# Kernel optimization log

Measured on AMD Instinct MI355X. Metric: run time of the kernel, lower is better.

Reference implementation:

```python
import jax, jax.numpy as jnp
import numpy as np

N_NODES = 100000
N_EDGES = 1600000
C = 64       # in_channels == filters
K = 3        # Chebyshev order
EPS = 1e-5   # InstanceNorm eps


def setup_inputs() -> dict:
    key = jax.random.key(0)
    ks = jax.random.split(key, 8)
    x = jax.random.normal(ks[0], (N_NODES, C), dtype=jnp.float32)
    edge_index = jax.random.randint(ks[1], (2, N_EDGES), 0, N_NODES, dtype=jnp.int64)
    scale = 1.0 / np.sqrt(C)
    W1 = jax.random.normal(ks[2], (K, C, C), dtype=jnp.float32) * scale
    b1 = jnp.zeros((C,), dtype=jnp.float32)
    W2 = jax.random.normal(ks[3], (K, C, C), dtype=jnp.float32) * scale
    b2 = jnp.zeros((C,), dtype=jnp.float32)
    return {"x": x, "edge_index": edge_index, "W1": W1, "b1": b1, "W2": W2, "b2": b2}


def _cheb_conv(x, src, dst, w_edge, W, b, n):
    # PyG ChebConv, norm='sym', lambda_max=2: L_hat = -D^{-1/2} A D^{-1/2}
    def prop(h):  # h: [N, C] -> L_hat @ h via gather -> weight -> scatter-add
        return jax.ops.segment_sum(w_edge[:, None] * h[src], dst, num_segments=n)
    Tx0 = x
    Tx1 = prop(x)
    Tx2 = 2.0 * prop(Tx1) - Tx0
    return Tx0 @ W[0] + Tx1 @ W[1] + Tx2 @ W[2] + b


def _instance_norm(h):
    # PyG InstanceNorm (single graph, affine=False): normalize over nodes per channel
    m = h.mean(axis=0, keepdims=True)
    v = h.var(axis=0, keepdims=True)
    return (h - m) * jax.lax.rsqrt(v + EPS)


def reference(x, edge_index, W1, b1, W2, b2):
    n = x.shape[0]
    src, dst = edge_index[0], edge_index[1]
    ones = jnp.ones((src.shape[0],), dtype=x.dtype)
    deg = jax.ops.segment_sum(ones, dst, num_segments=n)
    safe = jnp.where(deg > 0, deg, 1.0)
    dinv = jnp.where(deg > 0, jax.lax.rsqrt(safe), 0.0)
    w_edge = -dinv[src] * dinv[dst]  # scaled-Laplacian edge weights
    h = _instance_norm(jax.nn.relu(_cheb_conv(x, src, dst, w_edge, W1, b1, n)))
    h = _instance_norm(jax.nn.relu(_cheb_conv(h, src, dst, w_edge, W2, b2, n)))
    return h
```

## Files before the change

### kernel.cpp

```cpp
#include <hip/hip_runtime.h>
#include <hip/hip_fp16.h>

#define NCH 64
#define EPS 1e-5f
#define SBANKS 32
#define BSHIFT 8
#define NHIST 256
#define BINCAP 6400
#define SRCMASK 0x1FFFFu
#define QW_SCALE 32767.0f
#define QW_INV (1.0f/32767.0f)

typedef _Float16 f16x8 __attribute__((ext_vector_type(8)));
typedef float f32x4 __attribute__((ext_vector_type(4)));

__global__ __launch_bounds__(256) void k_front(const float* __restrict__ x, __half* __restrict__ xh,
                                               int castTotal, int castB,
                                               const float* __restrict__ W1, _Float16* __restrict__ Wb1,
                                               const float* __restrict__ W2, _Float16* __restrict__ Wb2,
                                               const int* __restrict__ dst, int* __restrict__ cnt,
                                               int E, int per, int nbuck) {
    int bid = blockIdx.x;
    if (bid < castB) {
        int i = (bid * 256 + threadIdx.x) * 4;
        if (i < castTotal) {
            float4 f = *(const float4*)(x + i);
            __half2* o = (__half2*)(xh + i);
            o[0] = __floats2half2_rn(f.x, f.y);
            o[1] = __floats2half2_rn(f.z, f.w);
        }
        return;
    }
    if (bid < castB + 96) {
        int wb = bid - castB;
        const float* W = (wb < 48) ? W1 : W2;
        _Float16* Wb = (wb < 48) ? Wb1 : Wb2;
        int idx = (wb % 48) * 256 + threadIdx.x;
        int j = idx & 7;
        int lane = (idx >> 3) & 63;
        int tk = idx >> 9;
        int tile = tk / 6, kk = tk % 6;
        int k = kk * 32 + (lane >> 4) * 8 + j;
        int n = tile * 16 + (lane & 15);
        Wb[idx] = (_Float16)W[k * 64 + n];
        return;
    }
    __shared__ int lh[512];
    int hb = bid - castB - 96;
    for (int t = threadIdx.x; t < nbuck; t += 256) lh[t] = 0;
    __syncthreads();
    int lo = hb * per, hi = min(E, lo + per);
    for (int e = lo + threadIdx.x; e < hi; e += 256)
        atomicAdd(&lh[dst[e] >> BSHIFT], 1);
    __syncthreads();
    for (int t = threadIdx.x; t < nbuck; t += 256)
        if (lh[t]) atomicAdd(&cnt[t], lh[t]);
}

__global__ void k_bscan(const int* __restrict__ cnt, int* __restrict__ gbase,
                        int* __restrict__ gcur, int nbuck, int E) {
    __shared__ int s[512];
    int t = threadIdx.x;
    int v = (t < nbuck) ? cnt[t] : 0;
    s[t] = v;
    __syncthreads();
    for (int off = 1; off < 512; off <<= 1) {
        int add = (t >= off) ? s[t - off] : 0;
        __syncthreads();
        s[t] += add;
        __syncthreads();
    }
    if (t < nbuck) { int ex = s[t] - v; gbase[t] = ex; gcur[t] = ex; }
    if (t == 0) gbase[nbuck] = E;
}

__global__ __launch_bounds__(256) void k_bin(const int* __restrict__ src,
                                             const int* __restrict__ dst,
                                             int* __restrict__ gcur,
                                             int2* __restrict__ binned, int E, int per, int nbuck) {
    __shared__ int lh[512];
    __shared__ int lsc[512];
    __shared__ int lbase[512];
    __shared__ int lcur[512];
    __shared__ int2 sedge[BINCAP];
    int t = threadIdx.x;
    for (int i = t; i < 512; i += 256) lh[i] = 0;
    __syncthreads();
    int lo = blockIdx.x * per, hi = min(E, lo + per);
    for (int e = lo + t; e < hi; e += 256)
        atomicAdd(&lh[dst[e] >> BSHIFT], 1);
    __syncthreads();
    int v0 = lh[t], v1 = lh[t + 256];
    lsc[t] = v0; lsc[t + 256] = v1;
    __syncthreads();
    for (int off = 1; off < 512; off <<= 1) {
        int a0 = (t >= off) ? lsc[t - off] : 0;
        int a1 = (t + 256 >= off) ? lsc[t + 256 - off] : 0;
        __syncthreads();
        lsc[t] += a0; lsc[t + 256] += a1;
        __syncthreads();
    }
    lsc[t] -= v0; lsc[t + 256] -= v1;
    if (t < nbuck && v0) lbase[t] = atomicAdd(&gcur[t], v0);
    if (t + 256 < nbuck && v1) lbase[t + 256] = atomicAdd(&gcur[t + 256], v1);
    lcur[t] = lsc[t]; lcur[t + 256] = lsc[t + 256];
    __syncthreads();
    for (int e = lo + t; e < hi; e += 256) {
        int d = dst[e];
        int b = d >> BSHIFT;
        int pos = atomicAdd(&lcur[b], 1);
        sedge[pos] = make_int2(src[e], d);
    }
    __syncthreads();
    int cntE = hi - lo;
    for (int i = t; i < cntE; i += 256) {
        int2 sd = sedge[i];
        int b = sd.y >> BSHIFT;
        binned[lbase[b] + (i - lsc[b])] = sd;
    }
}

__global__ __launch_bounds__(256) void k_bucket(const int2* __restrict__ binned,
                                                const int* __restrict__ gbase,
                                                float* __restrict__ dinv,
                                                int* __restrict__ rowstart,
                                                unsigned int* __restrict__ csr, int N, int nbuck, int E) {
    __shared__ int hist[256];
    __shared__ int lcur[256];
    __shared__ int ltmp[256];
    int b = blockIdx.x;
    int t = threadIdx.x;
    int nodeLo = b << BSHIFT;
    int nHere = min(256, N - nodeLo);
    int e0 = gbase[b], e1 = gbase[b + 1];
    hist[t] = 0;
    __syncthreads();
    for (int e = e0 + t; e < e1; e += 256)
        atomicAdd(&hist[binned[e].y - nodeLo], 1);
    __syncthreads();
    int deg = (t < nHere) ? hist[t] : 0;
    if (t < nHere) dinv[nodeLo + t] = (deg > 0) ? rsqrtf((float)deg) : 0.0f;
    ltmp[t] = deg;
    __syncthreads();
    for (int off = 1; off < 256; off <<= 1) {
        int add = (t >= off) ? ltmp[t - off] : 0;
        __syncthreads();
        ltmp[t] += add;
        __syncthreads();
    }
    int lstart = ltmp[t] - deg;
    if (t < nHere) rowstart[nodeLo + t] = e0 + lstart;
    if (b == nbuck - 1 && t == 0) rowstart[N] = E;
    lcur[t] = lstart;
    __syncthreads();
    for (int e = e0 + t; e < e1; e += 256) {
        int2 sd = binned[e];
        int dl = sd.y - nodeLo;
        int pos = atomicAdd(&lcur[dl], 1);
        unsigned int dd = (unsigned int)min(hist[dl], 32767);
        csr[e0 + pos] = (unsigned int)sd.x | (dd << 17);
    }
}

__global__ void k_weights(unsigned int* __restrict__ csr, const float* __restrict__ dinv, int E) {
    int e = blockIdx.x * blockDim.x + threadIdx.x;
    if (e < E) {
        unsigned int v = csr[e];
        unsigned int s = v & SRCMASK;
        float dd = rsqrtf((float)(v >> 17));
        float aw = dinv[s] * dd;
        unsigned int qw = (unsigned int)(aw * QW_SCALE + 0.5f);
        csr[e] = s | (qw << 17);
    }
}

__device__ __forceinline__ void edge_acc(const __half* __restrict__ h, unsigned int v,
                                         int li, float& sw, float (&acc)[8]) {
    uint4 a = *(const uint4*)(h + (size_t)(v & SRCMASK) * NCH + li * 8);
    float w = -(float)(v >> 17) * QW_INV;
    sw += w;
    float2 f;
    f = __half22float2(*(__half2*)&a.x); acc[0] = fmaf(w, f.x, acc[0]); acc[1] = fmaf(w, f.y, acc[1]);
    f = __half22float2(*(__half2*)&a.y); acc[2] = fmaf(w, f.x, acc[2]); acc[3] = fmaf(w, f.y, acc[3]);
    f = __half22float2(*(__half2*)&a.z); acc[4] = fmaf(w, f.x, acc[4]); acc[5] = fmaf(w, f.y, acc[5]);
    f = __half22float2(*(__half2*)&a.w); acc[6] = fmaf(w, f.x, acc[6]); acc[7] = fmaf(w, f.y, acc[7]);
}

__global__ __launch_bounds__(256) void k_prop(const __half* __restrict__ h,
                                              const int* __restrict__ rowstart,
                                              const unsigned int* __restrict__ csr,
                                              const __half* __restrict__ tx0,
                                              __half* __restrict__ y, int N,
                                              const float* __restrict__ gstats,
                                              const float* __restrict__ tstats) {
    int lane = threadIdx.x & 63;
    int wv = (blockIdx.x * 256 + threadIdx.x) >> 6;
    int g = lane >> 3, li = lane & 7;
    int node = wv * 8 + g;
    int e = 0, e1 = 0;
    if (node < N) { e = rowstart[node]; e1 = rowstart[node + 1]; }
    float acc[8] = {0.f, 0.f, 0.f, 0.f, 0.f, 0.f, 0.f, 0.f};
    float sw = 0.0f;
    for (; e + 4 <= e1; e += 4) {
        unsigned int v0 = csr[e], v1 = csr[e + 1], v2 = csr[e + 2], v3 = csr[e + 3];
        uint4 a0 = *(const uint4*)(h + (size_t)(v0 & SRCMASK) * NCH + li * 8);
        uint4 a1 = *(const uint4*)(h + (size_t)(v1 & SRCMASK) * NCH + li * 8);
        uint4 a2 = *(const uint4*)(h + (size_t)(v2 & SRCMASK) * NCH + li * 8);
        uint4 a3 = *(const uint4*)(h + (size_t)(v3 & SRCMASK) * NCH + li * 8);
        float w0 = -(float)(v0 >> 17) * QW_INV;
        float w1 = -(float)(v1 >> 17) * QW_INV;
        float w2 = -(float)(v2 >> 17) * QW_INV;
        float w3 = -(float)(v3 >> 17) * QW_INV;
        sw += (w0 + w1) + (w2 + w3);
        float2 f;
        f = __half22float2(*(__half2*)&a0.x); acc[0] = fmaf(w0, f.x, acc[0]); acc[1] = fmaf(w0, f.y, acc[1]);
        f = __half22float2(*(__half2*)&a0.y); acc[2] = fmaf(w0, f.x, acc[2]); acc[3] = fmaf(w0, f.y, acc[3]);
        f = __half22float2(*(__half2*)&a0.z); acc[4] = fmaf(w0, f.x, acc[4]); acc[5] = fmaf(w0, f.y, acc[5]);
        f = __half22float2(*(__half2*)&a0.w); acc[6] = fmaf(w0, f.x, acc[6]); acc[7] = fmaf(w0, f.y, acc[7]);
        f = __half22float2(*(__half2*)&a1.x); acc[0] = fmaf(w1, f.x, acc[0]); acc[1] = fmaf(w1, f.y, acc[1]);
        f = __half22float2(*(__half2*)&a1.y); acc[2] = fmaf(w1, f.x, acc[2]); acc[3] = fmaf(w1, f.y, acc[3]);
        f = __half22float2(*(__half2*)&a1.z); acc[4] = fmaf(w1, f.x, acc[4]); acc[5] = fmaf(w1, f.y, acc[5]);
        f = __half22float2(*(__half2*)&a1.w); acc[6] = fmaf(w1, f.x, acc[6]); acc[7] = fmaf(w1, f.y, acc[7]);
        f = __half22float2(*(__half2*)&a2.x); acc[0] = fmaf(w2, f.x, acc[0]); acc[1] = fmaf(w2, f.y, acc[1]);
        f = __half22float2(*(__half2*)&a2.y); acc[2] = fmaf(w2, f.x, acc[2]); acc[3] = fmaf(w2, f.y, acc[3]);
        f = __half22float2(*(__half2*)&a2.z); acc[4] = fmaf(w2, f.x, acc[4]); acc[5] = fmaf(w2, f.y, acc[5]);
        f = __half22float2(*(__half2*)&a2.w); acc[6] = fmaf(w2, f.x, acc[6]); acc[7] = fmaf(w2, f.y, acc[7]);
        f = __half22float2(*(__half2*)&a3.x); acc[0] = fmaf(w3, f.x, acc[0]); acc[1] = fmaf(w3, f.y, acc[1]);
        f = __half22float2(*(__half2*)&a3.y); acc[2] = fmaf(w3, f.x, acc[2]); acc[3] = fmaf(w3, f.y, acc[3]);
        f = __half22float2(*(__half2*)&a3.z); acc[4] = fmaf(w3, f.x, acc[4]); acc[5] = fmaf(w3, f.y, acc[5]);
        f = __half22float2(*(__half2*)&a3.w); acc[6] = fmaf(w3, f.x, acc[6]); acc[7] = fmaf(w3, f.y, acc[7]);
    }
    for (; e < e1; e++) {
        unsigned int v = csr[e];
        edge_acc(h, v, li, sw, acc);
    }
    if (node >= N) return;
    if (gstats != nullptr) {
        float4 m0 = *(const float4*)(gstats + li * 8);
        float4 m1 = *(const float4*)(gstats + li * 8 + 4);
        float4 r0 = *(const float4*)(gstats + 64 + li * 8);
        float4 r1 = *(const float4*)(gstats + 64 + li * 8 + 4);
        acc[0] = r0.x * (acc[0] - m0.x * sw);
        acc[1] = r0.y * (acc[1] - m0.y * sw);
        acc[2] = r0.z * (acc[2] - m0.z * sw);
        acc[3] = r0.w * (acc[3] - m0.w * sw);
        acc[4] = r1.x * (acc[4] - m1.x * sw);
        acc[5] = r1.y * (acc[5] - m1.y * sw);
        acc[6] = r1.z * (acc[6] - m1.z * sw);
        acc[7] = r1.w * (acc[7] - m1.w * sw);
    }
    if (tx0 != nullptr) {
        uint4 tq = *(const uint4*)(tx0 + (size_t)node * NCH + li * 8);
        float tv[8];
        float2 f;
        f = __half22float2(*(__half2*)&tq.x); tv[0] = f.x; tv[1] = f.y;
        f = __half22float2(*(__half2*)&tq.y); tv[2] = f.x; tv[3] = f.y;
        f = __half22float2(*(__half2*)&tq.z); tv[4] = f.x; tv[5] = f.y;
        f = __half22float2(*(__half2*)&tq.w); tv[6] = f.x; tv[7] = f.y;
        if (tstats != nullptr) {
            float4 m0 = *(const float4*)(tstats + li * 8);
            float4 m1 = *(const float4*)(tstats + li * 8 + 4);
            float4 r0 = *(const float4*)(tstats + 64 + li * 8);
            float4 r1 = *(const float4*)(tstats + 64 + li * 8 + 4);
            tv[0] = (tv[0] - m0.x) * r0.x; tv[1] = (tv[1] - m0.y) * r0.y;
            tv[2] = (tv[2] - m0.z) * r0.z; tv[3] = (tv[3] - m0.w) * r0.w;
            tv[4] = (tv[4] - m1.x) * r1.x; tv[5] = (tv[5] - m1.y) * r1.y;
            tv[6] = (tv[6] - m1.z) * r1.z; tv[7] = (tv[7] - m1.w) * r1.w;
        }
#pragma unroll
        for (int j = 0; j < 8; j++) acc[j] = 2.0f * acc[j] - tv[j];
    }
    uint4 o;
    __half2 hh;
    hh = __floats2half2_rn(acc[0], acc[1]); o.x = *(unsigned int*)&hh;
    hh = __floats2half2_rn(acc[2], acc[3]); o.y = *(unsigned int*)&hh;
    hh = __floats2half2_rn(acc[4], acc[5]); o.z = *(unsigned int*)&hh;
    hh = __floats2half2_rn(acc[6], acc[7]); o.w = *(unsigned int*)&hh;
    *(uint4*)(y + (size_t)node * NCH + li * 8) = o;
}

template <typename TOUT>
__global__ __launch_bounds__(256) void k_dmm(const __half* __restrict__ tx0,
                                             const __half* __restrict__ tx1,
                                             const __half* __restrict__ tx2,
                                             const _Float16* __restrict__ Wb,
                                             const float* __restrict__ b,
                                             TOUT* __restrict__ out,
                                             float* __restrict__ statsP, int N,
                                             const float* __restrict__ tstats) {
    __shared__ float sred[64];
    __shared__ float sq[64];
    int t = threadIdx.x;
    int w = t >> 6;
    int lane = t & 63;
    if (t < 64) { sred[t] = 0.f; sq[t] = 0.f; }
    __syncthreads();

    int nb16 = blockIdx.x * 64 + w * 16;
    int m = lane & 15, q = lane >> 4;
    int row = nb16 + m;
    int rowC = (row < N) ? row : 0;
    const __half* base0 = tx0 + (size_t)rowC * NCH;
    const __half* base1 = tx1 + (size_t)rowC * NCH;
    const __half* base2 = tx2 + (size_t)rowC * NCH;

    f32x4 acc[4];
#pragma unroll
    for (int tile = 0; tile < 4; tile++) acc[tile] = (f32x4){0.f, 0.f, 0.f, 0.f};

#pragma unroll
    for (int kk = 0; kk < 6; kk++) {
        const __half* ap = (kk < 2 ? base0 : (kk < 4 ? base1 : base2)) + (kk & 1) * 32 + q * 8;
        f16x8 a = *(const f16x8*)ap;
        if (kk < 2 && tstats != nullptr) {
            int cbase = (kk & 1) * 32 + q * 8;
#pragma unroll
            for (int j = 0; j < 8; j++) {
                float v = (float)a[j];
                a[j] = (_Float16)((v - tstats[cbase + j]) * tstats[64 + cbase + j]);
            }
        }
#pragma unroll
        for (int tile = 0; tile < 4; tile++) {
            f16x8 bf = *(const f16x8*)(Wb + ((size_t)(tile * 6 + kk) * 64 + lane) * 8);
            acc[tile] = __builtin_amdgcn_mfma_f32_16x16x32_f16(a, bf, acc[tile], 0, 0, 0);
        }
    }

#pragma unroll
    for (int tile = 0; tile < 4; tile++) {
        int ch = tile * 16 + m;
        float bb = b[ch];
        float s = 0.f, qq = 0.f;
#pragma unroll
        for (int r = 0; r < 4; r++) {
            int node = nb16 + q * 4 + r;
            float v = fmaxf(acc[tile][r] + bb, 0.f);
            if (node < N) {
                out[(size_t)node * NCH + ch] = (TOUT)v;
                s += v;
                qq = fmaf(v, v, qq);
            }
        }
        s += __shfl_xor(s, 16, 64);  s += __shfl_xor(s, 32, 64);
        qq += __shfl_xor(qq, 16, 64); qq += __shfl_xor(qq, 32, 64);
        if (q == 0) { atomicAdd(&sred[ch], s); atomicAdd(&sq[ch], qq); }
    }
    __syncthreads();
    if (t < 64) {
        int bank = blockIdx.x & (SBANKS - 1);
        atomicAdd(&statsP[bank * 128 + t], sred[t]);
        atomicAdd(&statsP[bank * 128 + 64 + t], sq[t]);
    }
}

__global__ void k_final(float* __restrict__ statsP, float invN) {
    int c = threadIdx.x;
    float S = 0.f, Q = 0.f;
    for (int k = 0; k < SBANKS; k++) {
        S += statsP[k * 128 + c];
        Q += statsP[k * 128 + 64 + c];
    }
    float m = S * invN;
    float var = Q * invN - m * m;
    statsP[SBANKS * 128 + c] = m;
    statsP[SBANKS * 128 + 64 + c] = rsqrtf(var + EPS);
}

__global__ void k_norm_hf(const __half* __restrict__ a, float* __restrict__ o,
                          const float* __restrict__ statsP, int total) {
    int i = blockIdx.x * blockDim.x + threadIdx.x;
    if (i >= total) return;
    int lane = i & 63;
    o[i] = (__half2float(a[i]) - statsP[SBANKS * 128 + lane]) * statsP[SBANKS * 128 + 64 + lane];
}

extern "C" void kernel_launch(void* const* d_in, const int* in_sizes, int n_in,
                              void* d_out, int out_size, void* d_ws, size_t ws_size,
                              hipStream_t stream) {
    const float* x  = (const float*)d_in[0];
    const int*   ei = (const int*)d_in[1];
    const float* W1 = (const float*)d_in[2];
    const float* b1 = (const float*)d_in[3];
    const float* W2 = (const float*)d_in[4];
    const float* b2 = (const float*)d_in[5];
    float* out = (float*)d_out;

    const int N = in_sizes[0] / NCH;
    const int E = in_sizes[1] / 2;
    const int* src = ei;
    const int* dst = ei + E;
    const int nbuck = (N + 255) >> BSHIFT;

    char* p = (char*)d_ws;
    auto alloc = [&](size_t bytes) {
        void* r = (void*)p;
        p += ((bytes + 255) / 256) * 256;
        return r;
    };
    float*  dinv     = (float*)alloc((size_t)N * 4);
    int*    rowstart = (int*)alloc((size_t)(N + 1) * 4);
    int*    cnt      = (int*)alloc((size_t)nbuck * 4);
    int*    gbase    = (int*)alloc((size_t)(nbuck + 1) * 4);
    int*    gcur     = (int*)alloc((size_t)nbuck * 4);
    unsigned int* csr = (unsigned int*)alloc((size_t)E * 4);
    __half* xh       = (__half*)alloc((size_t)N * NCH * 2);
    __half* Tx1      = (__half*)alloc((size_t)N * NCH * 2);
    __half* Tx2      = (__half*)alloc((size_t)N * NCH * 2);
    __half* A        = (__half*)alloc((size_t)N * NCH * 2);
    __half* A2       = (__half*)alloc((size_t)N * NCH * 2);
    _Float16* Wb1    = (_Float16*)alloc(12288 * 2);
    _Float16* Wb2    = (_Float16*)alloc(12288 * 2);
    const int statsFloats = SBANKS * 128 + 128;
    float*  stats    = (float*)alloc((size_t)2 * statsFloats * 4);
    float*  stats1 = stats;
    float*  stats2 = stats + statsFloats;
    const float* nrm1 = stats1 + SBANKS * 128;

    int2* binned = (int2*)Tx1;

    hipMemsetAsync(cnt, 0, (size_t)nbuck * 4, stream);
    hipMemsetAsync(stats, 0, (size_t)2 * statsFloats * 4, stream);

    const int TB = 256;
    int nbin = (E + BINCAP - 1) / BINCAP;
    if (nbin < 256) nbin = 256;
    const int perBin = (E + nbin - 1) / nbin;
    const int perH = (E + NHIST - 1) / NHIST;
    const int castTotal = N * NCH;
    const int castB = (castTotal / 4 + TB - 1) / TB;
    k_front<<<castB + 96 + NHIST, TB, 0, stream>>>(x, xh, castTotal, castB,
                                                   W1, Wb1, W2, Wb2,
                                                   dst, cnt, E, perH, nbuck);
    k_bscan<<<1, 512, 0, stream>>>(cnt, gbase, gcur, nbuck, E);
    k_bin<<<nbin, TB, 0, stream>>>(src, dst, gcur, binned, E, perBin, nbuck);
    k_bucket<<<nbuck, TB, 0, stream>>>(binned, gbase, dinv, rowstart, csr, N, nbuck, E);
    k_weights<<<(E + TB - 1) / TB, TB, 0, stream>>>(csr, dinv, E);

    const int propWaves = (N + 7) / 8;
    const int propBlocks = (propWaves + 3) / 4;
    const int dmmBlocks = (N + 63) / 64;
    const int normBlocks = (N * NCH + TB - 1) / TB;
    const float invN = 1.0f / (float)N;

    k_prop<<<propBlocks, TB, 0, stream>>>(xh, rowstart, csr, nullptr, Tx1, N, nullptr, nullptr);
    k_prop<<<propBlocks, TB, 0, stream>>>(Tx1, rowstart, csr, xh, Tx2, N, nullptr, nullptr);
    k_dmm<__half><<<dmmBlocks, TB, 0, stream>>>(xh, Tx1, Tx2, Wb1, b1, A, stats1, N, nullptr);
    k_final<<<1, 64, 0, stream>>>(stats1, invN);

    k_prop<<<propBlocks, TB, 0, stream>>>(A, rowstart, csr, nullptr, Tx1, N, nrm1, nullptr);
    k_prop<<<propBlocks, TB, 0, stream>>>(Tx1, rowstart, csr, A, Tx2, N, nullptr, nrm1);
    k_dmm<__half><<<dmmBlocks, TB, 0, stream>>>(A, Tx1, Tx2, Wb2, b2, A2, stats2, N, nrm1);
    k_final<<<1, 64, 0, stream>>>(stats2, invN);
    k_norm_hf<<<normBlocks, TB, 0, stream>>>(A2, out, stats2, N * NCH);
}
```

Measured before the change: 341.2 us.

## Pad CSR rows to multiples of eight for vectorized gather loop

Each node's CSR row is padded to a multiple of eight entries, with the padding holding zero-weight copies of a real neighbour, and each row is described by a (start, padded length) pair. The prop kernel then loads edge words as two uint4 vectors and processes eight neighbours per iteration with no scalar tail loop. This removes the tail-loop divergence and makes the index loads wider. In exchange the CSR grows and padding entries cost extra gathers. The two memsets are also merged into one.

```diff
diff --git a/kernel.cpp b/kernel.cpp
--- a/kernel.cpp
+++ b/kernel.cpp
@@ -7,6 +7,7 @@
 #define BSHIFT 8
 #define NHIST 256
 #define BINCAP 6400
+#define PADRES 2048
 #define SRCMASK 0x1FFFFu
 #define QW_SCALE 32767.0f
 #define QW_INV (1.0f/32767.0f)
@@ -123,8 +124,8 @@
 __global__ __launch_bounds__(256) void k_bucket(const int2* __restrict__ binned,
                                                 const int* __restrict__ gbase,
                                                 float* __restrict__ dinv,
-                                                int* __restrict__ rowstart,
-                                                unsigned int* __restrict__ csr, int N, int nbuck, int E) {
+                                                int2* __restrict__ rowinfo,
+                                                unsigned int* __restrict__ csr, int N, int nbuck) {
     __shared__ int hist[256];
     __shared__ int lcur[256];
     __shared__ int ltmp[256];
@@ -133,14 +134,16 @@
     int nodeLo = b << BSHIFT;
     int nHere = min(256, N - nodeLo);
     int e0 = gbase[b], e1 = gbase[b + 1];
+    int pb = (gbase[b] + b * PADRES + 7) & ~7;
     hist[t] = 0;
     __syncthreads();
     for (int e = e0 + t; e < e1; e += 256)
         atomicAdd(&hist[binned[e].y - nodeLo], 1);
     __syncthreads();
     int deg = (t < nHere) ? hist[t] : 0;
+    int pdeg = (deg + 7) & ~7;
     if (t < nHere) dinv[nodeLo + t] = (deg > 0) ? rsqrtf((float)deg) : 0.0f;
-    ltmp[t] = deg;
+    ltmp[t] = pdeg;
     __syncthreads();
     for (int off = 1; off < 256; off <<= 1) {
         int add = (t >= off) ? ltmp[t - off] : 0;
@@ -148,9 +151,8 @@
         ltmp[t] += add;
         __syncthreads();
     }
-    int lstart = ltmp[t] - deg;
-    if (t < nHere) rowstart[nodeLo + t] = e0 + lstart;
-    if (b == nbuck - 1 && t == 0) rowstart[N] = E;
+    int lstart = ltmp[t] - pdeg;
+    if (t < nHere) rowinfo[nodeLo + t] = make_int2(pb + lstart, pdeg);
     lcur[t] = lstart;
     __syncthreads();
     for (int e = e0 + t; e < e1; e += 256) {
@@ -158,36 +160,30 @@
         int dl = sd.y - nodeLo;
         int pos = atomicAdd(&lcur[dl], 1);
         unsigned int dd = (unsigned int)min(hist[dl], 32767);
-        csr[e0 + pos] = (unsigned int)sd.x | (dd << 17);
-    }
-}
-
-__global__ void k_weights(unsigned int* __restrict__ csr, const float* __restrict__ dinv, int E) {
+        csr[pb + pos] = (unsigned int)sd.x | (dd << 17);
+    }
+    __syncthreads();
+    if (t < nHere && pdeg > deg) {
+        unsigned int fill = (deg > 0) ? (csr[pb + lstart] & SRCMASK) : 0u;
+        for (int i = deg; i < pdeg; i++) csr[pb + lstart + i] = fill;
+    }
+}
+
+__global__ void k_weights(unsigned int* __restrict__ csr, const float* __restrict__ dinv, int PE) {
     int e = blockIdx.x * blockDim.x + threadIdx.x;
-    if (e < E) {
+    if (e < PE) {
         unsigned int v = csr[e];
+        unsigned int d = v >> 17;
+        if (d == 0) return;
         unsigned int s = v & SRCMASK;
-        float dd = rsqrtf((float)(v >> 17));
-        float aw = dinv[s] * dd;
+        float aw = dinv[s] * rsqrtf((float)d);
         unsigned int qw = (unsigned int)(aw * QW_SCALE + 0.5f);
         csr[e] = s | (qw << 17);
     }
 }
 
-__device__ __forceinline__ void edge_acc(const __half* __restrict__ h, unsigned int v,
-                                         int li, float& sw, float (&acc)[8]) {
-    uint4 a = *(const uint4*)(h + (size_t)(v & SRCMASK) * NCH + li * 8);
-    float w = -(float)(v >> 17) * QW_INV;
-    sw += w;
-    float2 f;
-    f = __half22float2(*(__half2*)&a.x); acc[0] = fmaf(w, f.x, acc[0]); acc[1] = fmaf(w, f.y, acc[1]);
-    f = __half22float2(*(__half2*)&a.y); acc[2] = fmaf(w, f.x, acc[2]); acc[3] = fmaf(w, f.y, acc[3]);
-    f = __half22float2(*(__half2*)&a.z); acc[4] = fmaf(w, f.x, acc[4]); acc[5] = fmaf(w, f.y, acc[5]);
-    f = __half22float2(*(__half2*)&a.w); acc[6] = fmaf(w, f.x, acc[6]); acc[7] = fmaf(w, f.y, acc[7]);
-}
-
 __global__ __launch_bounds__(256) void k_prop(const __half* __restrict__ h,
-                                              const int* __restrict__ rowstart,
+                                              const int2* __restrict__ rowinfo,
                                               const unsigned int* __restrict__ csr,
                                               const __half* __restrict__ tx0,
                                               __half* __restrict__ y, int N,
@@ -198,20 +194,34 @@
     int g = lane >> 3, li = lane & 7;
     int node = wv * 8 + g;
     int e = 0, e1 = 0;
-    if (node < N) { e = rowstart[node]; e1 = rowstart[node + 1]; }
+    if (node < N) {
+        int2 info = rowinfo[node];
+        e = info.x;
+        e1 = info.x + info.y;
+    }
     float acc[8] = {0.f, 0.f, 0.f, 0.f, 0.f, 0.f, 0.f, 0.f};
     float sw = 0.0f;
-    for (; e + 4 <= e1; e += 4) {
-        unsigned int v0 = csr[e], v1 = csr[e + 1], v2 = csr[e + 2], v3 = csr[e + 3];
-        uint4 a0 = *(const uint4*)(h + (size_t)(v0 & SRCMASK) * NCH + li * 8);
-        uint4 a1 = *(const uint4*)(h + (size_t)(v1 & SRCMASK) * NCH + li * 8);
-        uint4 a2 = *(const uint4*)(h + (size_t)(v2 & SRCMASK) * NCH + li * 8);
-        uint4 a3 = *(const uint4*)(h + (size_t)(v3 & SRCMASK) * NCH + li * 8);
-        float w0 = -(float)(v0 >> 17) * QW_INV;
-        float w1 = -(float)(v1 >> 17) * QW_INV;
-        float w2 = -(float)(v2 >> 17) * QW_INV;
-        float w3 = -(float)(v3 >> 17) * QW_INV;
-        sw += (w0 + w1) + (w2 + w3);
+    const __half* hb = h + li * 8;
+    for (; e < e1; e += 8) {
+        uint4 c0 = *(const uint4*)(csr + e);
+        uint4 c1 = *(const uint4*)(csr + e + 4);
+        uint4 a0 = *(const uint4*)(hb + (size_t)(c0.x & SRCMASK) * NCH);
+        uint4 a1 = *(const uint4*)(hb + (size_t)(c0.y & SRCMASK) * NCH);
+        uint4 a2 = *(const uint4*)(hb + (size_t)(c0.z & SRCMASK) * NCH);
+        uint4 a3 = *(const uint4*)(hb + (size_t)(c0.w & SRCMASK) * NCH);
+        uint4 a4 = *(const uint4*)(hb + (size_t)(c1.x & SRCMASK) * NCH);
+        uint4 a5 = *(const uint4*)(hb + (size_t)(c1.y & SRCMASK) * NCH);
+        uint4 a6 = *(const uint4*)(hb + (size_t)(c1.z & SRCMASK) * NCH);
+        uint4 a7 = *(const uint4*)(hb + (size_t)(c1.w & SRCMASK) * NCH);
+        float w0 = -(float)(c0.x >> 17) * QW_INV;
+        float w1 = -(float)(c0.y >> 17) * QW_INV;
+        float w2 = -(float)(c0.z >> 17) * QW_INV;
+        float w3 = -(float)(c0.w >> 17) * QW_INV;
+        float w4 = -(float)(c1.x >> 17) * QW_INV;
+        float w5 = -(float)(c1.y >> 17) * QW_INV;
+        float w6 = -(float)(c1.z >> 17) * QW_INV;
+        float w7 = -(float)(c1.w >> 17) * QW_INV;
+        sw += ((w0 + w1) + (w2 + w3)) + ((w4 + w5) + (w6 + w7));
         float2 f;
         f = __half22float2(*(__half2*)&a0.x); acc[0] = fmaf(w0, f.x, acc[0]); acc[1] = fmaf(w0, f.y, acc[1]);
         f = __half22float2(*(__half2*)&a0.y); acc[2] = fmaf(w0, f.x, acc[2]); acc[3] = fmaf(w0, f.y, acc[3]);
@@ -229,10 +239,22 @@
         f = __half22float2(*(__half2*)&a3.y); acc[2] = fmaf(w3, f.x, acc[2]); acc[3] = fmaf(w3, f.y, acc[3]);
         f = __half22float2(*(__half2*)&a3.z); acc[4] = fmaf(w3, f.x, acc[4]); acc[5] = fmaf(w3, f.y, acc[5]);
         f = __half22float2(*(__half2*)&a3.w); acc[6] = fmaf(w3, f.x, acc[6]); acc[7] = fmaf(w3, f.y, acc[7]);
-    }
-    for (; e < e1; e++) {
-        unsigned int v = csr[e];
-        edge_acc(h, v, li, sw, acc);
+        f = __half22float2(*(__half2*)&a4.x); acc[0] = fmaf(w4, f.x, acc[0]); acc[1] = fmaf(w4, f.y, acc[1]);
+        f = __half22float2(*(__half2*)&a4.y); acc[2] = fmaf(w4, f.x, acc[2]); acc[3] = fmaf(w4, f.y, acc[3]);
+        f = __half22float2(*(__half2*)&a4.z); acc[4] = fmaf(w4, f.x, acc[4]); acc[5] = fmaf(w4, f.y, acc[5]);
+        f = __half22float2(*(__half2*)&a4.w); acc[6] = fmaf(w4, f.x, acc[6]); acc[7] = fmaf(w4, f.y, acc[7]);
+        f = __half22float2(*(__half2*)&a5.x); acc[0] = fmaf(w5, f.x, acc[0]); acc[1] = fmaf(w5, f.y, acc[1]);
+        f = __half22float2(*(__half2*)&a5.y); acc[2] = fmaf(w5, f.x, acc[2]); acc[3] = fmaf(w5, f.y, acc[3]);
+        f = __half22float2(*(__half2*)&a5.z); acc[4] = fmaf(w5, f.x, acc[4]); acc[5] = fmaf(w5, f.y, acc[5]);
+        f = __half22float2(*(__half2*)&a5.w); acc[6] = fmaf(w5, f.x, acc[6]); acc[7] = fmaf(w5, f.y, acc[7]);
+        f = __half22float2(*(__half2*)&a6.x); acc[0] = fmaf(w6, f.x, acc[0]); acc[1] = fmaf(w6, f.y, acc[1]);
+        f = __half22float2(*(__half2*)&a6.y); acc[2] = fmaf(w6, f.x, acc[2]); acc[3] = fmaf(w6, f.y, acc[3]);
+        f = __half22float2(*(__half2*)&a6.z); acc[4] = fmaf(w6, f.x, acc[4]); acc[5] = fmaf(w6, f.y, acc[5]);
+        f = __half22float2(*(__half2*)&a6.w); acc[6] = fmaf(w6, f.x, acc[6]); acc[7] = fmaf(w6, f.y, acc[7]);
+        f = __half22float2(*(__half2*)&a7.x); acc[0] = fmaf(w7, f.x, acc[0]); acc[1] = fmaf(w7, f.y, acc[1]);
+        f = __half22float2(*(__half2*)&a7.y); acc[2] = fmaf(w7, f.x, acc[2]); acc[3] = fmaf(w7, f.y, acc[3]);
+        f = __half22float2(*(__half2*)&a7.z); acc[4] = fmaf(w7, f.x, acc[4]); acc[5] = fmaf(w7, f.y, acc[5]);
+        f = __half22float2(*(__half2*)&a7.w); acc[6] = fmaf(w7, f.x, acc[6]); acc[7] = fmaf(w7, f.y, acc[7]);
     }
     if (node >= N) return;
     if (gstats != nullptr) {
@@ -391,6 +413,7 @@
     const int* src = ei;
     const int* dst = ei + E;
     const int nbuck = (N + 255) >> BSHIFT;
+    const int PE = E + nbuck * PADRES + 8;
 
     char* p = (char*)d_ws;
     auto alloc = [&](size_t bytes) {
@@ -398,12 +421,9 @@
         p += ((bytes + 255) / 256) * 256;
         return r;
     };
-    float*  dinv     = (float*)alloc((size_t)N * 4);
-    int*    rowstart = (int*)alloc((size_t)(N + 1) * 4);
-    int*    cnt      = (int*)alloc((size_t)nbuck * 4);
-    int*    gbase    = (int*)alloc((size_t)(nbuck + 1) * 4);
-    int*    gcur     = (int*)alloc((size_t)nbuck * 4);
-    unsigned int* csr = (unsigned int*)alloc((size_t)E * 4);
+    float*  dinv     = (float*)alloc((size_t)131072 * 4);
+    int2*   rowinfo  = (int2*)alloc((size_t)N * 8);
+    unsigned int* csr = (unsigned int*)alloc((size_t)PE * 4);
     __half* xh       = (__half*)alloc((size_t)N * NCH * 2);
     __half* Tx1      = (__half*)alloc((size_t)N * NCH * 2);
     __half* Tx2      = (__half*)alloc((size_t)N * NCH * 2);
@@ -411,16 +431,17 @@
     __half* A2       = (__half*)alloc((size_t)N * NCH * 2);
     _Float16* Wb1    = (_Float16*)alloc(12288 * 2);
     _Float16* Wb2    = (_Float16*)alloc(12288 * 2);
+    int*    gbase    = (int*)alloc((size_t)(nbuck + 1) * 4);
+    int*    gcur     = (int*)alloc((size_t)nbuck * 4);
     const int statsFloats = SBANKS * 128 + 128;
-    float*  stats    = (float*)alloc((size_t)2 * statsFloats * 4);
-    float*  stats1 = stats;
-    float*  stats2 = stats + statsFloats;
+    int*    cnt      = (int*)alloc((size_t)nbuck * 4 + (size_t)2 * statsFloats * 4);
+    float*  stats1   = (float*)(cnt + nbuck);
+    float*  stats2   = stats1 + statsFloats;
     const float* nrm1 = stats1 + SBANKS * 128;
 
     int2* binned = (int2*)Tx1;
 
-    hipMemsetAsync(cnt, 0, (size_t)nbuck * 4, stream);
-    hipMemsetAsync(stats, 0, (size_t)2 * statsFloats * 4, stream);
+    hipMemsetAsync(cnt, 0, (size_t)nbuck * 4 + (size_t)2 * statsFloats * 4, stream);
 
     const int TB = 256;
     int nbin = (E + BINCAP - 1) / BINCAP;
@@ -434,8 +455,8 @@
                                                    dst, cnt, E, perH, nbuck);
     k_bscan<<<1, 512, 0, stream>>>(cnt, gbase, gcur, nbuck, E);
     k_bin<<<nbin, TB, 0, stream>>>(src, dst, gcur, binned, E, perBin, nbuck);
-    k_bucket<<<nbuck, TB, 0, stream>>>(binned, gbase, dinv, rowstart, csr, N, nbuck, E);
-    k_weights<<<(E + TB - 1) / TB, TB, 0, stream>>>(csr, dinv, E);
+    k_bucket<<<nbuck, TB, 0, stream>>>(binned, gbase, dinv, rowinfo, csr, N, nbuck);
+    k_weights<<<(PE + TB - 1) / TB, TB, 0, stream>>>(csr, dinv, PE);
 
     const int propWaves = (N + 7) / 8;
     const int propBlocks = (propWaves + 3) / 4;
@@ -443,13 +464,13 @@
     const int normBlocks = (N * NCH + TB - 1) / TB;
     const float invN = 1.0f / (float)N;
 
-    k_prop<<<propBlocks, TB, 0, stream>>>(xh, rowstart, csr, nullptr, Tx1, N, nullptr, nullptr);
-    k_prop<<<propBlocks, TB, 0, stream>>>(Tx1, rowstart, csr, xh, Tx2, N, nullptr, nullptr);
+    k_prop<<<propBlocks, TB, 0, stream>>>(xh, rowinfo, csr, nullptr, Tx1, N, nullptr, nullptr);
+    k_prop<<<propBlocks, TB, 0, stream>>>(Tx1, rowinfo, csr, xh, Tx2, N, nullptr, nullptr);
     k_dmm<__half><<<dmmBlocks, TB, 0, stream>>>(xh, Tx1, Tx2, Wb1, b1, A, stats1, N, nullptr);
     k_final<<<1, 64, 0, stream>>>(stats1, invN);
 
-    k_prop<<<propBlocks, TB, 0, stream>>>(A, rowstart, csr, nullptr, Tx1, N, nrm1, nullptr);
-    k_prop<<<propBlocks, TB, 0, stream>>>(Tx1, rowstart, csr, A, Tx2, N, nullptr, nrm1);
+    k_prop<<<propBlocks, TB, 0, stream>>>(A, rowinfo, csr, nullptr, Tx1, N, nrm1, nullptr);
+    k_prop<<<propBlocks, TB, 0, stream>>>(Tx1, rowinfo, csr, A, Tx2, N, nullptr, nrm1);
     k_dmm<__half><<<dmmBlocks, TB, 0, stream>>>(A, Tx1, Tx2, Wb2, b2, A2, stats2, N, nrm1);
     k_final<<<1, 64, 0, stream>>>(stats2, invN);
     k_norm_hf<<<normBlocks, TB, 0, stream>>>(A2, out, stats2, N * NCH);
```

Measured after the change: 333.5 us. -2.3%, faster.
